# Optimization experiments

Measured on AMD Instinct MI355X. Metric: run time of the kernel, lower is better.

Reference implementation:

```python
import jax, jax.numpy as jnp
import numpy as np

N_NODES = 100000
N_EDGES = 1600000
D = 128
L = 2


def setup_inputs() -> dict:
    key = jax.random.key(0)
    ks = jax.random.split(key, 8)
    s = 1.0 / np.sqrt(D)
    return {
        "x": jax.random.normal(ks[0], (N_NODES, D), dtype=jnp.float32),
        "edge_index": jax.random.randint(ks[1], (2, N_EDGES), 0, N_NODES, dtype=jnp.int64),
        "edge_weight": jax.random.uniform(ks[2], (N_EDGES,), dtype=jnp.float32),
        "weight": jax.random.normal(ks[3], (L, D, D), dtype=jnp.float32) * s,
        "w_ih": jax.random.normal(ks[4], (3 * D, D), dtype=jnp.float32) * s,
        "w_hh": jax.random.normal(ks[5], (3 * D, D), dtype=jnp.float32) * s,
        "b_ih": jax.random.normal(ks[6], (3 * D,), dtype=jnp.float32) * s,
        "b_hh": jax.random.normal(ks[7], (3 * D,), dtype=jnp.float32) * s,
    }


def _gru_cell(m, h, w_ih, w_hh, b_ih, b_hh):
    # torch.nn.GRUCell: gates ordered (reset, update, new)
    gi = m @ w_ih.T + b_ih  # [N, 3D]
    gh = h @ w_hh.T + b_hh  # [N, 3D]
    i_r, i_z, i_n = jnp.split(gi, 3, axis=-1)
    h_r, h_z, h_n = jnp.split(gh, 3, axis=-1)
    r = jax.nn.sigmoid(i_r + h_r)
    z = jax.nn.sigmoid(i_z + h_z)
    n = jnp.tanh(i_n + r * h_n)
    return (1.0 - z) * n + z * h


def reference(x, edge_index, edge_weight, weight, w_ih, w_hh, b_ih, b_hh):
    src = edge_index[0]
    dst = edge_index[1]
    h = x  # in_channels == out_channels, no zero-padding needed
    for i in range(L):
        m = h @ weight[i]                          # [N, D]
        msg = m[src] * edge_weight[:, None]        # [E, D] gather + scale
        agg = jax.ops.segment_sum(msg, dst, num_segments=N_NODES)  # scatter-add
        h = _gru_cell(agg, h, w_ih, w_hh, b_ih, b_hh)
    return h
```

## Files before the change

### kernel.cpp

```cpp
#include <hip/hip_runtime.h>
#include <hip/hip_bf16.h>
#include <stdint.h>

typedef unsigned short u16;
typedef unsigned long long u64;
typedef __attribute__((ext_vector_type(8))) short bf16x8;
typedef __attribute__((ext_vector_type(4))) float f32x4;

#define DD 128
#define NB 256
#define SB 10240

__device__ __forceinline__ u16 f2bf(float f){
  uint32_t u = __float_as_uint(f);
  uint32_t r = (u + 0x7fffu + ((u >> 16) & 1u)) >> 16;
  return (u16)r;
}
__device__ __forceinline__ float bf2f(u16 h){ return __uint_as_float(((uint32_t)h) << 16); }

struct Frag2 { bf16x8 hi, lo; };

__device__ __forceinline__ Frag2 split8(float4 v0, float4 v1){
  union { float f[8]; uint32_t u[8]; } U;
  *(float4*)&U.f[0] = v0; *(float4*)&U.f[4] = v1;
  union { uint32_t w[4]; bf16x8 v; } H, L;
  #pragma unroll
  for (int q = 0; q < 4; q++){
    uint32_t a = U.u[2*q], b = U.u[2*q+1];
    H.w[q] = __builtin_amdgcn_perm(b, a, 0x07060302);
    float l0 = U.f[2*q]   - __uint_as_float(a & 0xffff0000u);
    float l1 = U.f[2*q+1] - __uint_as_float(b & 0xffff0000u);
    L.w[q] = __builtin_amdgcn_perm(__float_as_uint(l1), __float_as_uint(l0), 0x07060302);
  }
  Frag2 r; r.hi = H.v; r.lo = L.v; return r;
}

__device__ __forceinline__ Frag2 load_afrag_g(const float* A, int row, int k0){
  const float4* p = (const float4*)(A + (size_t)row * DD + k0);
  return split8(p[0], p[1]);
}

__global__ void pack_kernel(const float* __restrict__ w, const float* __restrict__ wih,
                            const float* __restrict__ whh, const float* __restrict__ bih,
                            const float* __restrict__ bhh, u16* __restrict__ wtb,
                            u16* __restrict__ ihb, u16* __restrict__ hhb,
                            float* __restrict__ bias, int* __restrict__ gcursor, int L){
  int tid = blockIdx.x * 256 + threadIdx.x;
  int lane = tid & 63;
  int b1 = L * 2048, b2 = b1 + 6144, b3 = b2 + 6144, b4 = b3 + 512, b5 = b4 + NB;
  if (tid < b1){
    int kc = (tid >> 6) & 3, t = (tid >> 8) & 7, l = tid >> 11;
    int col = t*16 + (lane & 15), kb = kc*32 + 8*(lane >> 4);
    #pragma unroll
    for (int e = 0; e < 8; e++)
      wtb[(size_t)tid*8 + e] = f2bf(w[(size_t)l*DD*DD + (size_t)(kb + e)*DD + col]);
  } else if (tid < b2){
    int id = tid - b1;
    int kc = (id >> 6) & 3, t = id >> 8;
    int row = t*16 + (lane & 15), kb = kc*32 + 8*(lane >> 4);
    #pragma unroll
    for (int e = 0; e < 8; e++)
      ihb[(size_t)id*8 + e] = f2bf(wih[(size_t)row*DD + kb + e]);
  } else if (tid < b3){
    int id = tid - b2;
    int kc = (id >> 6) & 3, t = id >> 8;
    int row = t*16 + (lane & 15), kb = kc*32 + 8*(lane >> 4);
    #pragma unroll
    for (int e = 0; e < 8; e++)
      hhb[(size_t)id*8 + e] = f2bf(whh[(size_t)row*DD + kb + e]);
  } else if (tid < b4){
    int id = tid - b3;
    if (id < 256)      bias[id] = bih[id] + bhh[id];
    else if (id < 384) bias[id] = bih[id];
    else               bias[id] = bhh[id - 128];
  } else if (tid < b5){
    gcursor[tid - b4] = 0;
  }
}

__global__ __launch_bounds__(256) void binA_kernel(const int* __restrict__ src,
    const int* __restrict__ dst, const float* __restrict__ ew,
    int* __restrict__ gcursor, u64* __restrict__ staging, int E, int N){
  __shared__ unsigned lcnt[NB];
  __shared__ unsigned lbase[NB];
  __shared__ unsigned lcur[NB];
  __shared__ unsigned gbase[NB];
  __shared__ unsigned char sbucket[4096];
  __shared__ u64 sedge[4096];
  const int CH = 4096;
  int tid = threadIdx.x;
  int e0 = blockIdx.x * CH;

  lcnt[tid] = 0;
  __syncthreads();
  for (int i = tid; i < CH; i += 256){
    int e = e0 + i;
    if (e < E){
      unsigned d = (unsigned)dst[e];
      if (d < (unsigned)N) atomicAdd(&lcnt[d >> 9], 1u);
    }
  }
  __syncthreads();
  lbase[tid] = lcnt[tid];
  __syncthreads();
  for (int off = 1; off < NB; off <<= 1){
    unsigned t = (tid >= off) ? lbase[tid - off] : 0u;
    __syncthreads();
    lbase[tid] += t;
    __syncthreads();
  }
  unsigned total = lbase[NB - 1];
  lbase[tid] -= lcnt[tid];
  gbase[tid] = (unsigned)atomicAdd(&gcursor[tid], (int)lcnt[tid]);
  lcur[tid] = lbase[tid];
  __syncthreads();
  for (int i = tid; i < CH; i += 256){
    int e = e0 + i;
    if (e < E){
      unsigned d = (unsigned)dst[e];
      if (d < (unsigned)N){
        unsigned b = d >> 9;
        unsigned p = atomicAdd(&lcur[b], 1u);
        unsigned s = (unsigned)src[e];
        sedge[p] = ((u64)__float_as_uint(ew[e]) << 32) | ((u64)(s & 0x1FFFFu) << 9)
                 | (u64)(d & 0x1FFu);
        sbucket[p] = (unsigned char)b;
      }
    }
  }
  __syncthreads();
  for (int i = tid; i < (int)total; i += 256){
    unsigned b = sbucket[i];
    unsigned gpos = gbase[b] + ((unsigned)i - lbase[b]);
    if (gpos < SB) staging[(size_t)b*SB + gpos] = sedge[i];
  }
}

__global__ __launch_bounds__(256) void binB_kernel(const u64* __restrict__ staging,
    const int* __restrict__ gcursor, int* __restrict__ row_ptr,
    uint2* __restrict__ entries, int N, int E){
  __shared__ int sg[NB];
  __shared__ unsigned ncnt[512];
  __shared__ unsigned nsc[512];
  __shared__ unsigned ncur[512];
  int tid = threadIdx.x;
  int b = blockIdx.x;
  sg[tid] = gcursor[tid];
  __syncthreads();
  for (int off = 1; off < NB; off <<= 1){
    int t = (tid >= off) ? sg[tid - off] : 0;
    __syncthreads();
    sg[tid] += t;
    __syncthreads();
  }
  int cnt = gcursor[b];
  if (cnt > SB) cnt = SB;
  int base = sg[b] - cnt;
  if (b == NB - 1 && tid == 0) row_ptr[N] = sg[NB - 1];
  const u64* st = staging + (size_t)b * SB;

  ncnt[tid] = 0; ncnt[tid + 256] = 0;
  __syncthreads();
  for (int i = tid; i < cnt; i += 256)
    atomicAdd(&ncnt[(unsigned)(st[i] & 0x1FFu)], 1u);
  __syncthreads();
  nsc[tid] = ncnt[tid]; nsc[tid + 256] = ncnt[tid + 256];
  __syncthreads();
  for (int off = 1; off < 512; off <<= 1){
    unsigned t0 = (tid >= off) ? nsc[tid - off] : 0u;
    unsigned t1 = (tid + 256 >= off) ? nsc[tid + 256 - off] : 0u;
    __syncthreads();
    nsc[tid] += t0; nsc[tid + 256] += t1;
    __syncthreads();
  }
  #pragma unroll
  for (int h = 0; h < 2; h++){
    int k = tid + h*256;
    unsigned excl = nsc[k] - ncnt[k];
    int g = b*512 + k;
    if (g < N) row_ptr[g] = base + (int)excl;
    ncur[k] = excl;
  }
  __syncthreads();
  for (int i = tid; i < cnt; i += 256){
    u64 v = st[i];
    unsigned local = (unsigned)(v & 0x1FFu);
    unsigned p = atomicAdd(&ncur[local], 1u);
    uint2 ent;
    ent.x = (unsigned)((v >> 9) & 0x1FFFFu);
    ent.y = (unsigned)(v >> 32);
    entries[base + p] = ent;
  }
}

__global__ __launch_bounds__(256) void gemm_m_kernel(const float* __restrict__ hin,
    const u16* __restrict__ wb, u16* __restrict__ mout, int nstripes){
  __shared__ u16 lw[32*512];
  int lane = threadIdx.x & 63;
  int wid = threadIdx.x >> 6;
  int stripe = blockIdx.x*4 + wid;
  bool active = stripe < nstripes;
  int n0 = (active ? stripe : (nstripes - 1)) * 16;
  int lrow = lane & 15, lk = lane >> 4;

  bf16x8 sreg[8];
  #pragma unroll
  for (int b = 0; b < 8; b++){
    int q = wid*8 + b;
    sreg[b] = *(const bf16x8*)(wb + ((size_t)q*64 + lane)*8);
  }
  Frag2 a[4];
  #pragma unroll
  for (int kc = 0; kc < 4; kc++)
    a[kc] = load_afrag_g(hin, n0 + lrow, kc*32 + 8*lk);
  #pragma unroll
  for (int b = 0; b < 8; b++){
    int q = wid*8 + b;
    *(bf16x8*)(lw + ((size_t)q*64 + lane)*8) = sreg[b];
  }
  __syncthreads();

  f32x4 zero = {0.f, 0.f, 0.f, 0.f};
  f32x4 acc[8];
  #pragma unroll
  for (int t = 0; t < 8; t++) acc[t] = zero;
  #pragma unroll
  for (int kc = 0; kc < 4; kc++){
    #pragma unroll
    for (int t = 0; t < 8; t++){
      bf16x8 b = *(const bf16x8*)(lw + ((size_t)(t*4 + kc)*64 + lane)*8);
      acc[t] = __builtin_amdgcn_mfma_f32_16x16x32_bf16(a[kc].hi, b, acc[t], 0, 0, 0);
      acc[t] = __builtin_amdgcn_mfma_f32_16x16x32_bf16(a[kc].lo, b, acc[t], 0, 0, 0);
    }
  }
  if (active){
    #pragma unroll
    for (int r = 0; r < 4; r++){
      #pragma unroll
      for (int t = 0; t < 8; t++)
        mout[(size_t)(n0 + lk*4 + r)*DD + t*16 + lrow] = f2bf(acc[t][r]);
    }
  }
}

__global__ __launch_bounds__(256) void gather_kernel(const int* __restrict__ row_ptr,
    const uint2* __restrict__ entries, const u16* __restrict__ mbf,
    float* __restrict__ agg, int N){
  int lane = threadIdx.x & 63;
  int q = lane >> 4;
  int t = lane & 15;
  int node = (blockIdx.x*256 + threadIdx.x) >> 6;
  if (node >= N) return;
  int s = row_ptr[node], e = row_ptr[node + 1];
  float acc[8];
  #pragma unroll
  for (int c = 0; c < 8; c++) acc[c] = 0.f;
  #pragma unroll 4
  for (int i = s; i < e; i += 4){
    int idx = i + q;
    bool valid = idx < e;
    uint2 en = entries[valid ? idx : i];
    float w = valid ? __uint_as_float(en.y) : 0.f;
    uint4 mv = *(const uint4*)(mbf + (size_t)en.x*DD + 8*t);
    acc[0] += w * __uint_as_float(mv.x << 16);
    acc[1] += w * __uint_as_float(mv.x & 0xffff0000u);
    acc[2] += w * __uint_as_float(mv.y << 16);
    acc[3] += w * __uint_as_float(mv.y & 0xffff0000u);
    acc[4] += w * __uint_as_float(mv.z << 16);
    acc[5] += w * __uint_as_float(mv.z & 0xffff0000u);
    acc[6] += w * __uint_as_float(mv.w << 16);
    acc[7] += w * __uint_as_float(mv.w & 0xffff0000u);
  }
  #pragma unroll
  for (int c = 0; c < 8; c++){
    acc[c] += __shfl_xor(acc[c], 16);
    acc[c] += __shfl_xor(acc[c], 32);
  }
  if (q == 0){
    float4 o0 = {acc[0], acc[1], acc[2], acc[3]};
    float4 o1 = {acc[4], acc[5], acc[6], acc[7]};
    *(float4*)(agg + (size_t)node*DD + 8*t)     = o0;
    *(float4*)(agg + (size_t)node*DD + 8*t + 4) = o1;
  }
}

__global__ __launch_bounds__(256, 4) void gru_kernel(
    const float* __restrict__ agg, const float* hin,
    const u16* __restrict__ ihb, const u16* __restrict__ hhb,
    const float* __restrict__ bias, float* hout, int nstripes){
  __shared__ u16 lw[2][12*512];
  int lane = threadIdx.x & 63;
  int wid = threadIdx.x >> 6;
  int stripe = blockIdx.x*4 + wid;
  bool active = stripe < nstripes;
  int n0 = (active ? stripe : (nstripes - 1)) * 16;
  int lrow = lane & 15, lk = lane >> 4;

  Frag2 aa[4], ahf[4];
  #pragma unroll
  for (int kc = 0; kc < 4; kc++){
    int k0 = kc*32 + 8*lk;
    aa[kc]  = load_afrag_g(agg, n0 + lrow, k0);
    ahf[kc] = load_afrag_g(hin, n0 + lrow, k0);
  }

  int q = wid*3;
  int g0 = q >> 2,       kc0 = q & 3;
  int g1 = (q+1) >> 2,   kc1 = (q+1) & 3;
  int g2 = (q+2) >> 2,   kc2 = (q+2) & 3;

  {
    bf16x8 s0 = *(const bf16x8*)(ihb + ((size_t)((g0*8 + 0)*4 + kc0)*64 + lane)*8);
    bf16x8 s1 = *(const bf16x8*)(ihb + ((size_t)((g1*8 + 0)*4 + kc1)*64 + lane)*8);
    bf16x8 s2 = *(const bf16x8*)(ihb + ((size_t)((g2*8 + 0)*4 + kc2)*64 + lane)*8);
    *(bf16x8*)(lw[0] + ((size_t)(q+0)*64 + lane)*8) = s0;
    *(bf16x8*)(lw[0] + ((size_t)(q+1)*64 + lane)*8) = s1;
    *(bf16x8*)(lw[0] + ((size_t)(q+2)*64 + lane)*8) = s2;
  }
  __syncthreads();

  f32x4 zero = {0.f, 0.f, 0.f, 0.f};
  f32x4 ir = zero, iz = zero, in_ = zero, hr = zero, hz = zero, hn = zero;
  for (int ph = 0; ph < 16; ph++){
    int jt = ph >> 1, half = ph & 1;
    bf16x8 n0r, n1r, n2r;
    if (ph < 15){
      int njt = (ph + 1) >> 1;
      const u16* wsrc = ((ph + 1) & 1) ? hhb : ihb;
      n0r = *(const bf16x8*)(wsrc + ((size_t)((g0*8 + njt)*4 + kc0)*64 + lane)*8);
      n1r = *(const bf16x8*)(wsrc + ((size_t)((g1*8 + njt)*4 + kc1)*64 + lane)*8);
      n2r = *(const bf16x8*)(wsrc + ((size_t)((g2*8 + njt)*4 + kc2)*64 + lane)*8);
    }
    const u16* buf = lw[ph & 1];
    if (half == 0){
      ir = zero; iz = zero; in_ = zero;
      #pragma unroll
      for (int kc = 0; kc < 4; kc++){
        bf16x8 b0 = *(const bf16x8*)(buf + ((size_t)(0*4 + kc)*64 + lane)*8);
        bf16x8 b1 = *(const bf16x8*)(buf + ((size_t)(1*4 + kc)*64 + lane)*8);
        bf16x8 b2 = *(const bf16x8*)(buf + ((size_t)(2*4 + kc)*64 + lane)*8);
        ir  = __builtin_amdgcn_mfma_f32_16x16x32_bf16(aa[kc].hi, b0, ir,  0, 0, 0);
        ir  = __builtin_amdgcn_mfma_f32_16x16x32_bf16(aa[kc].lo, b0, ir,  0, 0, 0);
        iz  = __builtin_amdgcn_mfma_f32_16x16x32_bf16(aa[kc].hi, b1, iz,  0, 0, 0);
        iz  = __builtin_amdgcn_mfma_f32_16x16x32_bf16(aa[kc].lo, b1, iz,  0, 0, 0);
        in_ = __builtin_amdgcn_mfma_f32_16x16x32_bf16(aa[kc].hi, b2, in_, 0, 0, 0);
        in_ = __builtin_amdgcn_mfma_f32_16x16x32_bf16(aa[kc].lo, b2, in_, 0, 0, 0);
      }
    } else {
      hr = zero; hz = zero; hn = zero;
      #pragma unroll
      for (int kc = 0; kc < 4; kc++){
        bf16x8 b0 = *(const bf16x8*)(buf + ((size_t)(0*4 + kc)*64 + lane)*8);
        bf16x8 b1 = *(const bf16x8*)(buf + ((size_t)(1*4 + kc)*64 + lane)*8);
        bf16x8 b2 = *(const bf16x8*)(buf + ((size_t)(2*4 + kc)*64 + lane)*8);
        hr = __builtin_amdgcn_mfma_f32_16x16x32_bf16(ahf[kc].hi, b0, hr, 0, 0, 0);
        hr = __builtin_amdgcn_mfma_f32_16x16x32_bf16(ahf[kc].lo, b0, hr, 0, 0, 0);
        hz = __builtin_amdgcn_mfma_f32_16x16x32_bf16(ahf[kc].hi, b1, hz, 0, 0, 0);
        hz = __builtin_amdgcn_mfma_f32_16x16x32_bf16(ahf[kc].lo, b1, hz, 0, 0, 0);
        hn = __builtin_amdgcn_mfma_f32_16x16x32_bf16(ahf[kc].hi, b2, hn, 0, 0, 0);
        hn = __builtin_amdgcn_mfma_f32_16x16x32_bf16(ahf[kc].lo, b2, hn, 0, 0, 0);
      }
      if (active){
        int j = jt*16 + lrow;
        float br = bias[j];
        float bz = bias[128 + j];
        float bi = bias[256 + j];
        float bh = bias[384 + j];
        #pragma unroll
        for (int r = 0; r < 4; r++){
          int node = n0 + lk*4 + r;
          float xr = ir[r] + hr[r] + br;
          float xz = iz[r] + hz[r] + bz;
          float rg = __builtin_amdgcn_rcpf(1.f + __expf(-xr));
          float zg = __builtin_amdgcn_rcpf(1.f + __expf(-xz));
          float xn = in_[r] + bi + rg*(hn[r] + bh);
          xn = fminf(fmaxf(xn, -30.f), 30.f);
          float e2 = __expf(2.f*xn);
          float ng = 1.f - 2.f*__builtin_amdgcn_rcpf(e2 + 1.f);
          float hv = hin[(size_t)node*DD + j];
          hout[(size_t)node*DD + j] = ng + zg*(hv - ng);
        }
      }
    }
    if (ph < 15){
      u16* nbuf = lw[(ph + 1) & 1];
      *(bf16x8*)(nbuf + ((size_t)(q+0)*64 + lane)*8) = n0r;
      *(bf16x8*)(nbuf + ((size_t)(q+1)*64 + lane)*8) = n1r;
      *(bf16x8*)(nbuf + ((size_t)(q+2)*64 + lane)*8) = n2r;
    }
    __syncthreads();
  }
}

extern "C" void kernel_launch(void* const* d_in, const int* in_sizes, int n_in,
                              void* d_out, int out_size, void* d_ws, size_t ws_size,
                              hipStream_t stream){
  const float* x   = (const float*)d_in[0];
  const int*   ei  = (const int*)d_in[1];
  const float* ew  = (const float*)d_in[2];
  const float* wgt = (const float*)d_in[3];
  const float* wih = (const float*)d_in[4];
  const float* whh = (const float*)d_in[5];
  const float* bih = (const float*)d_in[6];
  const float* bhh = (const float*)d_in[7];
  float* out = (float*)d_out;

  const int N = in_sizes[0] / DD;
  const int E = in_sizes[2];
  const int L = in_sizes[3] / (DD * DD);

  char* p = (char*)d_ws;
  auto alloc = [&](size_t b) -> char* {
    char* r = p; p += (b + 255) & ~(size_t)255; return r;
  };
  u16*   wtb     = (u16*)  alloc((size_t)L * 2048 * 8 * 2);
  u16*   ihb     = (u16*)  alloc((size_t)6144 * 8 * 2);
  u16*   hhb     = (u16*)  alloc((size_t)6144 * 8 * 2);
  float* bias    = (float*)alloc(512 * 4);
  int*   gcursor = (int*)  alloc(NB * 4);
  int*   row_ptr = (int*)  alloc(((size_t)N + 1) * 4);
  uint2* entries = (uint2*)alloc((size_t)E * 8);
  u16*   mbf     = (u16*)  alloc((size_t)N * DD * 2);
  float* agg     = (float*)alloc((size_t)N * DD * 4);
  u64*   staging = (u64*)agg;

  const int* src = ei;
  const int* dst = ei + E;

  int packN = L*2048 + 6144 + 6144 + 512 + NB;
  pack_kernel<<<(packN + 255)/256, 256, 0, stream>>>(wgt, wih, whh, bih, bhh,
                                                     wtb, ihb, hhb, bias, gcursor, L);
  binA_kernel<<<(E + 4095)/4096, 256, 0, stream>>>(src, dst, ew, gcursor, staging, E, N);
  binB_kernel<<<NB, 256, 0, stream>>>(staging, gcursor, row_ptr, entries, N, E);

  int nstripes = N / 16;
  int ggrid = (nstripes + 3) / 4;
  for (int l = 0; l < L; l++){
    const float* hin = (l == 0) ? x : out;
    gemm_m_kernel<<<ggrid, 256, 0, stream>>>(hin, wtb + (size_t)l*2048*8, mbf, nstripes);
    gather_kernel<<<(N*64 + 255)/256, 256, 0, stream>>>(row_ptr, entries, mbf, agg, N);
    gru_kernel<<<ggrid, 256, 0, stream>>>(agg, hin, ihb, hhb, bias, out, nstripes);
  }
}
```

Baseline: 352.5 us.

## Fold message weight into GRU input weights and gather bf16 hidden state

Reassociates (A h W) W_ih^T as A h (W W_ih^T), precomputing the combined weight per layer so the separate per-layer node GEMM kernel is dropped. The gather now reads a bf16 copy of h directly; layer 0 gets it from a conversion kernel and later layers get it written by the GRU epilogue. This removes one full GEMM pass and its read and write of N x D per layer. In exchange it adds a small weight-combination kernel, an x conversion pass, and extra rounding, since h is quantised to bf16 before aggregation and the combined weights are stored in bf16.

Result: faster. 333.7 us, median of 3 (-5.3%).

```diff
diff --git a/kernel.cpp b/kernel.cpp
--- a/kernel.cpp
+++ b/kernel.cpp
@@ -40,41 +40,58 @@
   return split8(p[0], p[1]);
 }
 
-__global__ void pack_kernel(const float* __restrict__ w, const float* __restrict__ wih,
-                            const float* __restrict__ whh, const float* __restrict__ bih,
-                            const float* __restrict__ bhh, u16* __restrict__ wtb,
-                            u16* __restrict__ ihb, u16* __restrict__ hhb,
-                            float* __restrict__ bias, int* __restrict__ gcursor, int L){
+__global__ void pack_kernel(const float* __restrict__ whh, const float* __restrict__ bih,
+                            const float* __restrict__ bhh, u16* __restrict__ hhb,
+                            float* __restrict__ bias, int* __restrict__ gcursor){
   int tid = blockIdx.x * 256 + threadIdx.x;
   int lane = tid & 63;
-  int b1 = L * 2048, b2 = b1 + 6144, b3 = b2 + 6144, b4 = b3 + 512, b5 = b4 + NB;
+  int b1 = 6144, b2 = b1 + 512, b3 = b2 + NB;
   if (tid < b1){
-    int kc = (tid >> 6) & 3, t = (tid >> 8) & 7, l = tid >> 11;
-    int col = t*16 + (lane & 15), kb = kc*32 + 8*(lane >> 4);
-    #pragma unroll
-    for (int e = 0; e < 8; e++)
-      wtb[(size_t)tid*8 + e] = f2bf(w[(size_t)l*DD*DD + (size_t)(kb + e)*DD + col]);
-  } else if (tid < b2){
-    int id = tid - b1;
-    int kc = (id >> 6) & 3, t = id >> 8;
+    int kc = (tid >> 6) & 3, t = tid >> 8;
     int row = t*16 + (lane & 15), kb = kc*32 + 8*(lane >> 4);
     #pragma unroll
     for (int e = 0; e < 8; e++)
-      ihb[(size_t)id*8 + e] = f2bf(wih[(size_t)row*DD + kb + e]);
-  } else if (tid < b3){
-    int id = tid - b2;
-    int kc = (id >> 6) & 3, t = id >> 8;
-    int row = t*16 + (lane & 15), kb = kc*32 + 8*(lane >> 4);
-    #pragma unroll
-    for (int e = 0; e < 8; e++)
-      hhb[(size_t)id*8 + e] = f2bf(whh[(size_t)row*DD + kb + e]);
-  } else if (tid < b4){
-    int id = tid - b3;
+      hhb[(size_t)tid*8 + e] = f2bf(whh[(size_t)row*DD + kb + e]);
+  } else if (tid < b2){
+    int id = tid - b1;
     if (id < 256)      bias[id] = bih[id] + bhh[id];
     else if (id < 384) bias[id] = bih[id];
     else               bias[id] = bhh[id - 128];
-  } else if (tid < b5){
-    gcursor[tid - b4] = 0;
+  } else if (tid < b3){
+    gcursor[tid - b2] = 0;
+  }
+}
+
+__global__ __launch_bounds__(256) void wc_kernel(const float* __restrict__ w,
+    const float* __restrict__ wih, u16* __restrict__ wcb, int L){
+  int tid = blockIdx.x*256 + threadIdx.x;
+  if (tid >= L*49152) return;
+  int l = tid / 49152;
+  int r = tid % 49152;
+  int k = r / 384;
+  int g = r % 384;
+  const float4* wr = (const float4*)(w + (size_t)l*DD*DD + (size_t)k*DD);
+  const float4* ir = (const float4*)(wih + (size_t)g*DD);
+  float acc = 0.f;
+  #pragma unroll
+  for (int j = 0; j < 32; j++){
+    float4 a = wr[j], b = ir[j];
+    acc += a.x*b.x + a.y*b.y + a.z*b.z + a.w*b.w;
+  }
+  int gate = g >> 7, c = g & 127;
+  int jt = c >> 4, lrow = c & 15;
+  int kc = k >> 5, sub = (k >> 3) & 3, e = k & 7;
+  wcb[(size_t)l*49152 + (size_t)(((gate*8 + jt)*4 + kc)*512 + (sub*16 + lrow)*8 + e)]
+      = f2bf(acc);
+}
+
+__global__ void conv_kernel(const float* __restrict__ x, u16* __restrict__ hb, int n4){
+  int i = blockIdx.x*256 + threadIdx.x;
+  if (i < n4){
+    float4 v = ((const float4*)x)[i];
+    ushort4 o;
+    o.x = f2bf(v.x); o.y = f2bf(v.y); o.z = f2bf(v.z); o.w = f2bf(v.w);
+    ((ushort4*)hb)[i] = o;
   }
 }
 
@@ -193,58 +210,8 @@
   }
 }
 
-__global__ __launch_bounds__(256) void gemm_m_kernel(const float* __restrict__ hin,
-    const u16* __restrict__ wb, u16* __restrict__ mout, int nstripes){
-  __shared__ u16 lw[32*512];
-  int lane = threadIdx.x & 63;
-  int wid = threadIdx.x >> 6;
-  int stripe = blockIdx.x*4 + wid;
-  bool active = stripe < nstripes;
-  int n0 = (active ? stripe : (nstripes - 1)) * 16;
-  int lrow = lane & 15, lk = lane >> 4;
-
-  bf16x8 sreg[8];
-  #pragma unroll
-  for (int b = 0; b < 8; b++){
-    int q = wid*8 + b;
-    sreg[b] = *(const bf16x8*)(wb + ((size_t)q*64 + lane)*8);
-  }
-  Frag2 a[4];
-  #pragma unroll
-  for (int kc = 0; kc < 4; kc++)
-    a[kc] = load_afrag_g(hin, n0 + lrow, kc*32 + 8*lk);
-  #pragma unroll
-  for (int b = 0; b < 8; b++){
-    int q = wid*8 + b;
-    *(bf16x8*)(lw + ((size_t)q*64 + lane)*8) = sreg[b];
-  }
-  __syncthreads();
-
-  f32x4 zero = {0.f, 0.f, 0.f, 0.f};
-  f32x4 acc[8];
-  #pragma unroll
-  for (int t = 0; t < 8; t++) acc[t] = zero;
-  #pragma unroll
-  for (int kc = 0; kc < 4; kc++){
-    #pragma unroll
-    for (int t = 0; t < 8; t++){
-      bf16x8 b = *(const bf16x8*)(lw + ((size_t)(t*4 + kc)*64 + lane)*8);
-      acc[t] = __builtin_amdgcn_mfma_f32_16x16x32_bf16(a[kc].hi, b, acc[t], 0, 0, 0);
-      acc[t] = __builtin_amdgcn_mfma_f32_16x16x32_bf16(a[kc].lo, b, acc[t], 0, 0, 0);
-    }
-  }
-  if (active){
-    #pragma unroll
-    for (int r = 0; r < 4; r++){
-      #pragma unroll
-      for (int t = 0; t < 8; t++)
-        mout[(size_t)(n0 + lk*4 + r)*DD + t*16 + lrow] = f2bf(acc[t][r]);
-    }
-  }
-}
-
 __global__ __launch_bounds__(256) void gather_kernel(const int* __restrict__ row_ptr,
-    const uint2* __restrict__ entries, const u16* __restrict__ mbf,
+    const uint2* __restrict__ entries, const u16* __restrict__ hb,
     float* __restrict__ agg, int N){
   int lane = threadIdx.x & 63;
   int q = lane >> 4;
@@ -261,7 +228,7 @@
     bool valid = idx < e;
     uint2 en = entries[valid ? idx : i];
     float w = valid ? __uint_as_float(en.y) : 0.f;
-    uint4 mv = *(const uint4*)(mbf + (size_t)en.x*DD + 8*t);
+    uint4 mv = *(const uint4*)(hb + (size_t)en.x*DD + 8*t);
     acc[0] += w * __uint_as_float(mv.x << 16);
     acc[1] += w * __uint_as_float(mv.x & 0xffff0000u);
     acc[2] += w * __uint_as_float(mv.y << 16);
@@ -286,8 +253,8 @@
 
 __global__ __launch_bounds__(256, 4) void gru_kernel(
     const float* __restrict__ agg, const float* hin,
-    const u16* __restrict__ ihb, const u16* __restrict__ hhb,
-    const float* __restrict__ bias, float* hout, int nstripes){
+    const u16* __restrict__ wcb, const u16* __restrict__ hhb,
+    const float* __restrict__ bias, float* hout, u16* hbout, int nstripes){
   __shared__ u16 lw[2][12*512];
   int lane = threadIdx.x & 63;
   int wid = threadIdx.x >> 6;
@@ -310,9 +277,9 @@
   int g2 = (q+2) >> 2,   kc2 = (q+2) & 3;
 
   {
-    bf16x8 s0 = *(const bf16x8*)(ihb + ((size_t)((g0*8 + 0)*4 + kc0)*64 + lane)*8);
-    bf16x8 s1 = *(const bf16x8*)(ihb + ((size_t)((g1*8 + 0)*4 + kc1)*64 + lane)*8);
-    bf16x8 s2 = *(const bf16x8*)(ihb + ((size_t)((g2*8 + 0)*4 + kc2)*64 + lane)*8);
+    bf16x8 s0 = *(const bf16x8*)(wcb + ((size_t)((g0*8 + 0)*4 + kc0)*64 + lane)*8);
+    bf16x8 s1 = *(const bf16x8*)(wcb + ((size_t)((g1*8 + 0)*4 + kc1)*64 + lane)*8);
+    bf16x8 s2 = *(const bf16x8*)(wcb + ((size_t)((g2*8 + 0)*4 + kc2)*64 + lane)*8);
     *(bf16x8*)(lw[0] + ((size_t)(q+0)*64 + lane)*8) = s0;
     *(bf16x8*)(lw[0] + ((size_t)(q+1)*64 + lane)*8) = s1;
     *(bf16x8*)(lw[0] + ((size_t)(q+2)*64 + lane)*8) = s2;
@@ -326,7 +293,7 @@
     bf16x8 n0r, n1r, n2r;
     if (ph < 15){
       int njt = (ph + 1) >> 1;
-      const u16* wsrc = ((ph + 1) & 1) ? hhb : ihb;
+      const u16* wsrc = ((ph + 1) & 1) ? hhb : wcb;
       n0r = *(const bf16x8*)(wsrc + ((size_t)((g0*8 + njt)*4 + kc0)*64 + lane)*8);
       n1r = *(const bf16x8*)(wsrc + ((size_t)((g1*8 + njt)*4 + kc1)*64 + lane)*8);
       n2r = *(const bf16x8*)(wsrc + ((size_t)((g2*8 + njt)*4 + kc2)*64 + lane)*8);
@@ -378,7 +345,9 @@
           float e2 = __expf(2.f*xn);
           float ng = 1.f - 2.f*__builtin_amdgcn_rcpf(e2 + 1.f);
           float hv = hin[(size_t)node*DD + j];
-          hout[(size_t)node*DD + j] = ng + zg*(hv - ng);
+          float val = ng + zg*(hv - ng);
+          hout[(size_t)node*DD + j] = val;
+          if (hbout) hbout[(size_t)node*DD + j] = f2bf(val);
         }
       }
     }
@@ -413,23 +382,23 @@
   auto alloc = [&](size_t b) -> char* {
     char* r = p; p += (b + 255) & ~(size_t)255; return r;
   };
-  u16*   wtb     = (u16*)  alloc((size_t)L * 2048 * 8 * 2);
-  u16*   ihb     = (u16*)  alloc((size_t)6144 * 8 * 2);
+  u16*   wcb     = (u16*)  alloc((size_t)L * 49152 * 2);
   u16*   hhb     = (u16*)  alloc((size_t)6144 * 8 * 2);
   float* bias    = (float*)alloc(512 * 4);
   int*   gcursor = (int*)  alloc(NB * 4);
   int*   row_ptr = (int*)  alloc(((size_t)N + 1) * 4);
   uint2* entries = (uint2*)alloc((size_t)E * 8);
-  u16*   mbf     = (u16*)  alloc((size_t)N * DD * 2);
+  u16*   hb      = (u16*)  alloc((size_t)N * DD * 2);
   float* agg     = (float*)alloc((size_t)N * DD * 4);
   u64*   staging = (u64*)agg;
 
   const int* src = ei;
   const int* dst = ei + E;
 
-  int packN = L*2048 + 6144 + 6144 + 512 + NB;
-  pack_kernel<<<(packN + 255)/256, 256, 0, stream>>>(wgt, wih, whh, bih, bhh,
-                                                     wtb, ihb, hhb, bias, gcursor, L);
+  int packN = 6144 + 512 + NB;
+  pack_kernel<<<(packN + 255)/256, 256, 0, stream>>>(whh, bih, bhh, hhb, bias, gcursor);
+  wc_kernel<<<(L*49152 + 255)/256, 256, 0, stream>>>(wgt, wih, wcb, L);
+  conv_kernel<<<(N*DD/4 + 255)/256, 256, 0, stream>>>(x, hb, N*DD/4);
   binA_kernel<<<(E + 4095)/4096, 256, 0, stream>>>(src, dst, ew, gcursor, staging, E, N);
   binB_kernel<<<NB, 256, 0, stream>>>(staging, gcursor, row_ptr, entries, N, E);
 
@@ -437,8 +406,8 @@
   int ggrid = (nstripes + 3) / 4;
   for (int l = 0; l < L; l++){
     const float* hin = (l == 0) ? x : out;
-    gemm_m_kernel<<<ggrid, 256, 0, stream>>>(hin, wtb + (size_t)l*2048*8, mbf, nstripes);
-    gather_kernel<<<(N*64 + 255)/256, 256, 0, stream>>>(row_ptr, entries, mbf, agg, N);
-    gru_kernel<<<ggrid, 256, 0, stream>>>(agg, hin, ihb, hhb, bias, out, nstripes);
-  }
-}
+    gather_kernel<<<(N*64 + 255)/256, 256, 0, stream>>>(row_ptr, entries, hb, agg, N);
+    gru_kernel<<<ggrid, 256, 0, stream>>>(agg, hin, wcb + (size_t)l*49152, hhb, bias,
+                                          out, (l == L - 1) ? nullptr : hb, nstripes);
+  }
+}
```
